# Performance work log

Measured on AMD Instinct MI355X. Metric: run time of the kernel, lower is better.

The kernel has to match this reference:

```python
import jax, jax.numpy as jnp
import numpy as np

B = 4096      # batch
D_IN = 512    # input_dim
D = 256       # d_model
T = 424       # n_targets
L = 6         # num_layers
EPS = 1e-5    # torch LayerNorm default


def _ln(x, g, b):
    m = jnp.mean(x, axis=-1, keepdims=True)
    v = jnp.var(x, axis=-1, keepdims=True)
    return (x - m) * jax.lax.rsqrt(v + EPS) * g + b


def setup_inputs() -> dict:
    key = jax.random.key(0)
    ks = iter(jax.random.split(key, 32))
    r = lambda shape, s=0.05: jax.random.normal(next(ks), shape, dtype=jnp.float32) * s
    return {
        'x': jax.random.normal(next(ks), (B, D_IN), dtype=jnp.float32),
        'proj_W': r((4, D // 4, D_IN)), 'proj_b': r((4, D // 4)),
        'attn_in_W': r((L, 3 * D, D)), 'attn_in_b': r((L, 3 * D)),
        'attn_out_W': r((L, D, D)), 'attn_out_b': r((L, D)),
        'ln_g': jnp.ones((L, D), jnp.float32), 'ln_b': jnp.zeros((L, D), jnp.float32),
        'ff_W1': r((L, 4 * D, D)), 'ff_b1': r((L, 4 * D)),
        'ff_W2': r((L, D, 4 * D)), 'ff_b2': r((L, D)),
        'cross_in_W': r((3 * D, D)), 'cross_in_b': r((3 * D,)),
        'cross_out_W': r((D, D)), 'cross_out_b': r((D,)),
        'tp_W1': r((T, D // 2, D)), 'tp_b1': r((T, D // 2)),
        'tp_ln_g': jnp.ones((T, D // 2), jnp.float32), 'tp_ln_b': jnp.zeros((T, D // 2), jnp.float32),
        'tp_W2': r((T, D // 4, D // 2)), 'tp_b2': r((T, D // 4)),
        'tp_W3': r((T, D // 4)), 'tp_b3': r((T,)),
    }


def reference(x, proj_W, proj_b, attn_in_W, attn_in_b, attn_out_W, attn_out_b,
              ln_g, ln_b, ff_W1, ff_b1, ff_W2, ff_b2,
              cross_in_W, cross_in_b, cross_out_W, cross_out_b,
              tp_W1, tp_b1, tp_ln_g, tp_ln_b, tp_W2, tp_b2, tp_W3, tp_b3):
    # 4 feature projections -> concat == reshape of stacked einsum  [B, 4, D/4] -> [B, D]
    h = jnp.einsum('bd,pkd->bpk', x, proj_W) + proj_b
    h = h.reshape(h.shape[0], D)

    # 6 transformer blocks on seq_len=1: softmax over a single key == 1, so
    # MHA(x,x,x) reduces exactly to out_proj(v_proj(x)); dropout = identity (eval).
    for i in range(L):
        Wv, bv = attn_in_W[i, 2 * D:], attn_in_b[i, 2 * D:]
        attn = (h @ Wv.T + bv) @ attn_out_W[i].T + attn_out_b[i]
        h = _ln(h + attn, ln_g[i], ln_b[i])          # same norm instance reused
        ff = jax.nn.gelu(h @ ff_W1[i].T + ff_b1[i], approximate=False) @ ff_W2[i].T + ff_b2[i]
        h = _ln(h + ff, ln_g[i], ln_b[i])

    # cross-target attention, also seq_len=1 -> v/out projections only
    Wv, bv = cross_in_W[2 * D:], cross_in_b[2 * D:]
    h = h + ((h @ Wv.T + bv) @ cross_out_W.T + cross_out_b)

    # 424 per-target MLP heads, batched as grouped GEMMs
    t = jnp.einsum('bd,tkd->btk', h, tp_W1) + tp_b1          # [B, T, 128]
    t = jax.nn.relu(_ln(t, tp_ln_g, tp_ln_b))
    t = jax.nn.relu(jnp.einsum('btk,tmk->btm', t, tp_W2) + tp_b2)  # [B, T, 64]
    out = jnp.einsum('btm,tm->bt', t, tp_W3) + tp_b3         # [B, T]
    return out
```

## Files before the change

kernel.cpp:

```cpp
#include <hip/hip_runtime.h>
#include <stdint.h>
#include <utility>
#include <type_traits>

using bf16x8 = __attribute__((ext_vector_type(8))) short;
using f32x4  = __attribute__((ext_vector_type(4))) float;

__device__ __forceinline__ f32x4 mfma16(bf16x8 a, bf16x8 b, f32x4 c) {
  return __builtin_amdgcn_mfma_f32_16x16x32_bf16(a, b, c, 0, 0, 0);
}

__device__ __forceinline__ unsigned short f2b_rne(float f) {
  union { float f; unsigned u; } v; v.f = f;
  unsigned r = v.u + 0x7fffu + ((v.u >> 16) & 1u);
  return (unsigned short)(r >> 16);
}

__device__ __forceinline__ void gload16(const void* g, void* l) {
  __builtin_amdgcn_global_load_lds(
      (const __attribute__((address_space(1))) void*)g,
      (__attribute__((address_space(3))) void*)l, 16, 0, 0);
}

template<int N> __device__ __forceinline__ void vmwait() {
  if constexpr (N <= 0)      asm volatile("s_waitcnt vmcnt(0)" ::: "memory");
  else if constexpr (N == 4) asm volatile("s_waitcnt vmcnt(4)" ::: "memory");
  else                       asm volatile("s_waitcnt vmcnt(8)" ::: "memory");
}

template<class F, int... Is>
__device__ __forceinline__ void sfor_impl(F&& f, std::integer_sequence<int, Is...>) {
  (f(std::integral_constant<int, Is>{}), ...);
}
template<int N, class F>
__device__ __forceinline__ void sfor(F&& f) {
  sfor_impl(static_cast<F&&>(f), std::make_integer_sequence<int, N>{});
}

__device__ __forceinline__ void stage_tile(const unsigned short* __restrict__ W, int K,
                                           int col0, int kt, char* slot, int lane) {
#pragma unroll
  for (int i = 0; i < 4; ++i) {
    const int chunk = i * 64 + lane;
    const int ci = chunk >> 4, kc = chunk & 15;
    const unsigned short* src = W + (size_t)(col0 + ci) * K + kt * 128
                                + (((kc * 16) ^ ((ci & 7) << 4)) >> 1);
    gload16(src, slot + i * 1024);
  }
}

template<int NCG, int NKT, int AS, int K>
__device__ __forceinline__ void gemm_pipe(const unsigned short* __restrict__ W, int c0,
                                          const char* __restrict__ abuf,
                                          char* __restrict__ ring, int lane,
                                          f32x4 (&acc)[NCG]) {
  const int r = lane & 15, hi16 = (lane >> 4) << 4;
  const int swz = (r & 7) << 4;
  constexpr int TILES = NCG * NKT;
  stage_tile(W, K, c0, 0, ring, lane);
  if constexpr (TILES > 1)
    stage_tile(W, K, c0 + (1 % NCG) * 16, 1 / NCG, ring + 4096, lane);
  bf16x8 areg[4];
  sfor<TILES>([&](auto tc) {
    constexpr int t = tc.value;
    constexpr int kt = t / NCG, cg = t % NCG;
    vmwait<((t + 2 <= TILES) ? 4 : 0)>();
    __builtin_amdgcn_sched_barrier(0);
    if constexpr (t + 2 < TILES) {
      constexpr int t2 = t + 2;
      stage_tile(W, K, c0 + (t2 % NCG) * 16, t2 / NCG, ring + (t2 % 3) * 4096, lane);
    }
    const char* slot = ring + (t % 3) * 4096;
#pragma unroll
    for (int ksl = 0; ksl < 4; ++ksl) {
      if constexpr (cg == 0)
        areg[ksl] = *reinterpret_cast<const bf16x8*>(
            abuf + r * AS + ((kt * 256 + ksl * 64 + hi16) ^ swz));
      const bf16x8 b = *reinterpret_cast<const bf16x8*>(
          slot + r * 256 + ((ksl * 64 + hi16) ^ swz));
      acc[cg] = mfma16(areg[ksl], b, acc[cg]);
    }
  });
}

__global__ void f2b_kernel(const float* __restrict__ s, unsigned short* __restrict__ d, int n4) {
  int i = blockIdx.x * 256 + threadIdx.x;
  if (i >= n4) return;
  float4 v = reinterpret_cast<const float4*>(s)[i];
  ushort4 o;
  o.x = f2b_rne(v.x); o.y = f2b_rne(v.y); o.z = f2b_rne(v.z); o.w = f2b_rne(v.w);
  reinterpret_cast<ushort4*>(d)[i] = o;
}

__global__ __launch_bounds__(256) void compose_attn(
    const float* __restrict__ aiW, const float* __restrict__ aib,
    const float* __restrict__ aoW, const float* __restrict__ aob,
    const float* __restrict__ ciW, const float* __restrict__ cib,
    const float* __restrict__ coW, const float* __restrict__ cob,
    unsigned short* __restrict__ wEff, float* __restrict__ bEff) {
  const int mat = blockIdx.y;
  const float* Wo = (mat < 6) ? aoW + (size_t)mat * 65536 : coW;
  const float* Wv = (mat < 6) ? aiW + (size_t)mat * 196608 + 131072 : ciW + 131072;
  const float* bv = (mat < 6) ? aib + mat * 768 + 512 : cib + 512;
  const float* bo = (mat < 6) ? aob + mat * 256 : cob;
  unsigned short* Wd = wEff + (size_t)mat * 65536;
  const int m = blockIdx.x * 16 + (threadIdx.x >> 4);
  const int k0 = (threadIdx.x & 15) * 16;
  float c[16] = {};
  for (int j = 0; j < 256; ++j) {
    const float a = Wo[m * 256 + j];
    const float* Br = Wv + j * 256 + k0;
#pragma unroll
    for (int kk = 0; kk < 16; ++kk) c[kk] = fmaf(a, Br[kk], c[kk]);
  }
#pragma unroll
  for (int kk = 0; kk < 16; ++kk) Wd[m * 256 + k0 + kk] = f2b_rne(c[kk]);
  if (blockIdx.x == 0) {
    const int mm = threadIdx.x;
    float s = 0.f;
    for (int j = 0; j < 256; ++j) s = fmaf(Wo[mm * 256 + j], bv[j], s);
    bEff[mat * 256 + mm] = s + bo[mm];
  }
}

__global__ __launch_bounds__(512, 2) void trunk_fused(
    const unsigned short* __restrict__ xb, const unsigned short* __restrict__ pWb,
    const float* __restrict__ projb,
    const unsigned short* __restrict__ wEff, const float* __restrict__ bEff,
    const unsigned short* __restrict__ f1Wb, const float* __restrict__ f1b,
    const unsigned short* __restrict__ f2Wb, const float* __restrict__ f2bp,
    const float* __restrict__ lng, const float* __restrict__ lnb,
    unsigned short* __restrict__ hbf) {
  __shared__ char hbuf[16 * 512];
  __shared__ char gbuf[16 * 2048];
  __shared__ char ringbuf[8 * 12288];
  __shared__ float red[2][16][8];
  const int tid = threadIdx.x, wid = tid >> 6, lane = tid & 63;
  const int r = lane & 15, hi = lane >> 4;
  const int swz = (r & 7) << 4;
  const int row0 = blockIdx.x << 4;
  const int colb = wid * 32;
  char* ring = ringbuf + wid * 12288;

#pragma unroll
  for (int i = 0; i < 2; ++i) {
    const int id = tid + i * 512, row = id >> 6, c8 = id & 63;
    bf16x8 v = *reinterpret_cast<const bf16x8*>(xb + (size_t)(row0 + row) * 512 + c8 * 8);
    *reinterpret_cast<bf16x8*>(gbuf + row * 1024 + ((c8 * 16) ^ ((row & 7) << 4))) = v;
  }
  __syncthreads();

  f32x4 hreg[2];

  auto store_hb = [&]() {
#pragma unroll
    for (int cf = 0; cf < 2; ++cf) {
      const int cb = (colb + cf * 16 + r) * 2;
#pragma unroll
      for (int j = 0; j < 4; ++j) {
        const int row = hi * 4 + j;
        *reinterpret_cast<unsigned short*>(hbuf + row * 512 + (cb ^ ((row & 7) << 4))) =
            f2b_rne(hreg[cf][j]);
      }
    }
  };

  auto ln_apply = [&](float gm0, float gm1, float bb0, float bb1) {
    float sum[4], sq[4];
#pragma unroll
    for (int j = 0; j < 4; ++j) {
      const float v0 = hreg[0][j], v1 = hreg[1][j];
      sum[j] = v0 + v1; sq[j] = v0 * v0 + v1 * v1;
    }
#pragma unroll
    for (int m = 1; m < 16; m <<= 1)
#pragma unroll
      for (int j = 0; j < 4; ++j) {
        sum[j] += __shfl_xor(sum[j], m, 64);
        sq[j]  += __shfl_xor(sq[j],  m, 64);
      }
    if (r == 0)
#pragma unroll
      for (int j = 0; j < 4; ++j) {
        red[0][hi * 4 + j][wid] = sum[j];
        red[1][hi * 4 + j][wid] = sq[j];
      }
    __syncthreads();
#pragma unroll
    for (int j = 0; j < 4; ++j) {
      const int row = hi * 4 + j;
      f32x4 p0 = *reinterpret_cast<const f32x4*>(&red[0][row][0]);
      f32x4 p1 = *reinterpret_cast<const f32x4*>(&red[0][row][4]);
      f32x4 q0 = *reinterpret_cast<const f32x4*>(&red[1][row][0]);
      f32x4 q1 = *reinterpret_cast<const f32x4*>(&red[1][row][4]);
      const float ts = p0[0]+p0[1]+p0[2]+p0[3]+p1[0]+p1[1]+p1[2]+p1[3];
      const float tq = q0[0]+q0[1]+q0[2]+q0[3]+q1[0]+q1[1]+q1[2]+q1[3];
      const float mean = ts * (1.f / 256.f);
      const float rstd = rsqrtf(tq * (1.f / 256.f) - mean * mean + 1e-5f);
      hreg[0][j] = (hreg[0][j] - mean) * rstd * gm0 + bb0;
      hreg[1][j] = (hreg[1][j] - mean) * rstd * gm1 + bb1;
    }
  };

  {
    f32x4 acc[2] = {};
    gemm_pipe<2, 4, 1024, 512>(pWb, colb, gbuf, ring, lane, acc);
    const float bv0 = projb[colb + r], bv1 = projb[colb + 16 + r];
#pragma unroll
    for (int j = 0; j < 4; ++j) { hreg[0][j] = acc[0][j] + bv0; hreg[1][j] = acc[1][j] + bv1; }
  }
  store_hb();
  __syncthreads();

  for (int L = 0; L < 6; ++L) {
    const float gm0 = lng[L * 256 + colb + r],      gm1 = lng[L * 256 + colb + 16 + r];
    const float bb0 = lnb[L * 256 + colb + r],      bb1 = lnb[L * 256 + colb + 16 + r];
    {
      f32x4 acc[2] = {};
      gemm_pipe<2, 2, 512, 256>(wEff + (size_t)L * 65536, colb, hbuf, ring, lane, acc);
      const float be0 = bEff[L * 256 + colb + r], be1 = bEff[L * 256 + colb + 16 + r];
#pragma unroll
      for (int j = 0; j < 4; ++j) { hreg[0][j] += acc[0][j] + be0; hreg[1][j] += acc[1][j] + be1; }
    }
    ln_apply(gm0, gm1, bb0, bb1);
    store_hb();
    __syncthreads();
    {
      f32x4 accf[8] = {};
      gemm_pipe<8, 2, 512, 256>(f1Wb + (size_t)L * 262144, wid * 128, hbuf, ring, lane, accf);
#pragma unroll
      for (int cf = 0; cf < 8; ++cf) {
        const int colw = wid * 128 + cf * 16 + r;
        const float bv = f1b[L * 1024 + colw];
        const int cb = colw * 2;
#pragma unroll
        for (int j = 0; j < 4; ++j) {
          float y = accf[cf][j] + bv;
          y = 0.5f * y * (1.f + erff(y * 0.70710678118654752f));
          const int row = hi * 4 + j;
          *reinterpret_cast<unsigned short*>(gbuf + row * 2048 + (cb ^ ((row & 7) << 4))) = f2b_rne(y);
        }
      }
    }
    __syncthreads();
    {
      f32x4 acc[2] = {};
      gemm_pipe<2, 8, 2048, 1024>(f2Wb + (size_t)L * 262144, colb, gbuf, ring, lane, acc);
      const float be0 = f2bp[L * 256 + colb + r], be1 = f2bp[L * 256 + colb + 16 + r];
#pragma unroll
      for (int j = 0; j < 4; ++j) { hreg[0][j] += acc[0][j] + be0; hreg[1][j] += acc[1][j] + be1; }
    }
    ln_apply(gm0, gm1, bb0, bb1);
    store_hb();
    __syncthreads();
  }

  {
    f32x4 acc[2] = {};
    gemm_pipe<2, 2, 512, 256>(wEff + 6ull * 65536, colb, hbuf, ring, lane, acc);
    const float be0 = bEff[1536 + colb + r], be1 = bEff[1536 + colb + 16 + r];
#pragma unroll
    for (int j = 0; j < 4; ++j) { hreg[0][j] += acc[0][j] + be0; hreg[1][j] += acc[1][j] + be1; }
  }
#pragma unroll
  for (int cf = 0; cf < 2; ++cf)
#pragma unroll
    for (int j = 0; j < 4; ++j)
      hbf[(size_t)(row0 + hi * 4 + j) * 256 + colb + cf * 16 + r] = f2b_rne(hreg[cf][j]);
}

__global__ __launch_bounds__(512, 2) void phase_d2(
    const unsigned short* __restrict__ hbf, const unsigned short* __restrict__ w1b,
    const float* __restrict__ b1, const float* __restrict__ lng, const float* __restrict__ lnb,
    const unsigned short* __restrict__ w2b, const float* __restrict__ b2,
    const float* __restrict__ w3, const float* __restrict__ b3,
    float* __restrict__ out) {
  __shared__ char sm[149504];
  const int tid = threadIdx.x, wid = tid >> 6, lane = tid & 63;
  const int r = lane & 15, hi = lane >> 4;
  const int sw = (r & 7) << 4;
  const int t = blockIdx.y;

  const unsigned short* w1t = w1b + (size_t)t * 32768;
  const unsigned short* w2t = w2b + (size_t)t * 8192;
#pragma unroll
  for (int i = 0; i < 8; ++i) {
    const int id = tid + i * 512;
    const int c = id >> 5, s = id & 31;
    bf16x8 v = *reinterpret_cast<const bf16x8*>(w1t + c * 256 + s * 8);
    *reinterpret_cast<bf16x8*>(sm + c * 512 + ((s * 16) ^ ((c & 7) << 4))) = v;
  }
#pragma unroll
  for (int i = 0; i < 2; ++i) {
    const int id = tid + i * 512;
    const int c = id >> 4, s = id & 15;
    bf16x8 v = *reinterpret_cast<const bf16x8*>(w2t + c * 128 + s * 8);
    *reinterpret_cast<bf16x8*>(sm + 65536 + c * 256 + ((s * 16) ^ ((c & 7) << 4))) = v;
  }
  {
    float v;
    if (tid < 128)      v = b1 [t * 128 + tid];
    else if (tid < 256) v = lng[t * 128 + tid - 128];
    else if (tid < 384) v = lnb[t * 128 + tid - 256];
    else if (tid < 448) v = b2 [t * 64  + tid - 384];
    else                v = w3 [t * 64  + tid - 448];
    reinterpret_cast<float*>(sm + 81920)[tid] = v;
  }
  __syncthreads();

  const float* cb1 = reinterpret_cast<const float*>(sm + 81920);
  const float* cg  = cb1 + 128;
  const float* cbe = cb1 + 256;
  const float* cb2 = cb1 + 384;
  const float* cw3 = cb1 + 448;
  char* t1w = sm + 83968 + wid * 8192;
  const float b3t = b3[t];
  const int token_b0 = blockIdx.x * 1024;

  for (int tile = 0; tile < 2; ++tile) {
    const int B0 = token_b0 + tile * 512 + wid * 64;

    f32x4 acc1[8][4] = {};
    bf16x8 bc[4], bn[4];
#pragma unroll
    for (int bf = 0; bf < 4; ++bf)
      bc[bf] = *reinterpret_cast<const bf16x8*>(hbf + (size_t)(B0 + bf * 16 + r) * 256 + hi * 8);
#pragma unroll
    for (int ks = 0; ks < 8; ++ks) {
      bf16x8 a[8];
#pragma unroll
      for (int cf = 0; cf < 8; ++cf)
        a[cf] = *reinterpret_cast<const bf16x8*>(sm + (cf * 16 + r) * 512 + ((ks * 64 + hi * 16) ^ sw));
      if (ks < 7) {
#pragma unroll
        for (int bf = 0; bf < 4; ++bf)
          bn[bf] = *reinterpret_cast<const bf16x8*>(hbf + (size_t)(B0 + bf * 16 + r) * 256 + (ks + 1) * 32 + hi * 8);
      }
#pragma unroll
      for (int cf = 0; cf < 8; ++cf)
#pragma unroll
        for (int bf = 0; bf < 4; ++bf)
          acc1[cf][bf] = mfma16(a[cf], bc[bf], acc1[cf][bf]);
#pragma unroll
      for (int bf = 0; bf < 4; ++bf) bc[bf] = bn[bf];
    }

#pragma unroll
    for (int cf = 0; cf < 8; ++cf) {
      f32x4 b1v = *reinterpret_cast<const f32x4*>(cb1 + cf * 16 + hi * 4);
#pragma unroll
      for (int bf = 0; bf < 4; ++bf) acc1[cf][bf] += b1v;
    }

    float mu[4], rsd[4];
#pragma unroll
    for (int bf = 0; bf < 4; ++bf) {
      float s = 0.f, s2 = 0.f;
#pragma unroll
      for (int cf = 0; cf < 8; ++cf)
#pragma unroll
        for (int j = 0; j < 4; ++j) { float v = acc1[cf][bf][j]; s += v; s2 += v * v; }
      s  += __shfl_xor(s, 16, 64);  s  += __shfl_xor(s, 32, 64);
      s2 += __shfl_xor(s2, 16, 64); s2 += __shfl_xor(s2, 32, 64);
      const float m = s * (1.f / 128.f);
      mu[bf] = m;
      rsd[bf] = rsqrtf(s2 * (1.f / 128.f) - m * m + 1e-5f);
    }

    f32x4 acc2[4][4] = {};
#pragma unroll
    for (int half = 0; half < 2; ++half) {
#pragma unroll
      for (int cf = 0; cf < 8; ++cf) {
        f32x4 gv = *reinterpret_cast<const f32x4*>(cg  + cf * 16 + hi * 4);
        f32x4 bv = *reinterpret_cast<const f32x4*>(cbe + cf * 16 + hi * 4);
#pragma unroll
        for (int bl = 0; bl < 2; ++bl) {
          const int bf = half * 2 + bl;
          unsigned o01, o23;
          {
            float y0 = fmaxf((acc1[cf][bf][0] - mu[bf]) * rsd[bf] * gv[0] + bv[0], 0.f);
            float y1 = fmaxf((acc1[cf][bf][1] - mu[bf]) * rsd[bf] * gv[1] + bv[1], 0.f);
            float y2 = fmaxf((acc1[cf][bf][2] - mu[bf]) * rsd[bf] * gv[2] + bv[2], 0.f);
            float y3 = fmaxf((acc1[cf][bf][3] - mu[bf]) * rsd[bf] * gv[3] + bv[3], 0.f);
            o01 = (unsigned)f2b_rne(y0) | ((unsigned)f2b_rne(y1) << 16);
            o23 = (unsigned)f2b_rne(y2) | ((unsigned)f2b_rne(y3) << 16);
          }
          uint2 pk; pk.x = o01; pk.y = o23;
          *reinterpret_cast<uint2*>(t1w + (bl * 16 + r) * 256 + ((cf * 32 + hi * 8) ^ sw)) = pk;
        }
      }
#pragma unroll
      for (int ks = 0; ks < 4; ++ks) {
        bf16x8 a2[4];
#pragma unroll
        for (int cf2 = 0; cf2 < 4; ++cf2)
          a2[cf2] = *reinterpret_cast<const bf16x8*>(sm + 65536 + (cf2 * 16 + r) * 256 + ((ks * 64 + hi * 16) ^ sw));
#pragma unroll
        for (int bl = 0; bl < 2; ++bl) {
          bf16x8 bb = *reinterpret_cast<const bf16x8*>(t1w + (bl * 16 + r) * 256 + ((ks * 64 + hi * 16) ^ sw));
#pragma unroll
          for (int cf2 = 0; cf2 < 4; ++cf2)
            acc2[cf2][half * 2 + bl] = mfma16(a2[cf2], bb, acc2[cf2][half * 2 + bl]);
        }
      }
    }

    float s[4] = {0.f, 0.f, 0.f, 0.f};
#pragma unroll
    for (int cf2 = 0; cf2 < 4; ++cf2) {
      f32x4 b2v = *reinterpret_cast<const f32x4*>(cb2 + cf2 * 16 + hi * 4);
      f32x4 w3v = *reinterpret_cast<const f32x4*>(cw3 + cf2 * 16 + hi * 4);
#pragma unroll
      for (int bf = 0; bf < 4; ++bf)
#pragma unroll
        for (int j = 0; j < 4; ++j)
          s[bf] += fmaxf(acc2[cf2][bf][j] + b2v[j], 0.f) * w3v[j];
    }
#pragma unroll
    for (int bf = 0; bf < 4; ++bf) {
      s[bf] += __shfl_xor(s[bf], 16, 64);
      s[bf] += __shfl_xor(s[bf], 32, 64);
      if (hi == 0) out[(size_t)(B0 + bf * 16 + r) * 424 + t] = s[bf] + b3t;
    }
  }
}

extern "C" void kernel_launch(void* const* d_in, const int* in_sizes, int n_in,
                              void* d_out, int out_size, void* d_ws, size_t ws_size,
                              hipStream_t stream) {
  const float* x     = (const float*)d_in[0];
  const float* projW = (const float*)d_in[1];
  const float* projb = (const float*)d_in[2];
  const float* aiW   = (const float*)d_in[3];
  const float* aib   = (const float*)d_in[4];
  const float* aoW   = (const float*)d_in[5];
  const float* aob   = (const float*)d_in[6];
  const float* lng   = (const float*)d_in[7];
  const float* lnbp  = (const float*)d_in[8];
  const float* f1W   = (const float*)d_in[9];
  const float* f1b   = (const float*)d_in[10];
  const float* f2W   = (const float*)d_in[11];
  const float* f2bp  = (const float*)d_in[12];
  const float* ciW   = (const float*)d_in[13];
  const float* cib   = (const float*)d_in[14];
  const float* coW   = (const float*)d_in[15];
  const float* cob   = (const float*)d_in[16];
  const float* tpW1  = (const float*)d_in[17];
  const float* tpb1  = (const float*)d_in[18];
  const float* tplng = (const float*)d_in[19];
  const float* tplnb = (const float*)d_in[20];
  const float* tpW2  = (const float*)d_in[21];
  const float* tpb2  = (const float*)d_in[22];
  const float* tpW3  = (const float*)d_in[23];
  const float* tpb3  = (const float*)d_in[24];
  float* out = (float*)d_out;

  char* ws = (char*)d_ws;
  size_t off = 0;
  auto alloc = [&](size_t n) { char* p = ws + off; off = (off + n + 255) & ~(size_t)255; return p; };
  unsigned short* xb   = (unsigned short*)alloc(4096ull * 512 * 2);
  unsigned short* pWb  = (unsigned short*)alloc(256ull * 512 * 2);
  unsigned short* f1Wb = (unsigned short*)alloc(6ull * 1024 * 256 * 2);
  unsigned short* f2Wb = (unsigned short*)alloc(6ull * 256 * 1024 * 2);
  unsigned short* W1b  = (unsigned short*)alloc(424ull * 128 * 256 * 2);
  unsigned short* W2b  = (unsigned short*)alloc(424ull * 64 * 128 * 2);
  unsigned short* wEff = (unsigned short*)alloc(7ull * 256 * 256 * 2);
  float*          bEff = (float*)alloc(7ull * 256 * 4);
  unsigned short* hbf  = (unsigned short*)alloc(4096ull * 256 * 2);

  auto conv = [&](const float* s, unsigned short* d, size_t n) {
    int n4 = (int)(n >> 2);
    f2b_kernel<<<dim3((n4 + 255) / 256), dim3(256), 0, stream>>>(s, d, n4);
  };
  compose_attn<<<dim3(16, 7), dim3(256), 0, stream>>>(aiW, aib, aoW, aob, ciW, cib, coW, cob, wEff, bEff);
  conv(x, xb, 4096ull * 512);
  conv(projW, pWb, 256ull * 512);
  conv(f1W, f1Wb, 6ull * 1024 * 256);
  conv(f2W, f2Wb, 6ull * 256 * 1024);
  conv(tpW1, W1b, 424ull * 128 * 256);
  conv(tpW2, W2b, 424ull * 64 * 128);

  trunk_fused<<<dim3(256), dim3(512), 0, stream>>>(
      xb, pWb, projb, wEff, bEff, f1Wb, f1b, f2Wb, f2bp, lng, lnbp, hbf);

  phase_d2<<<dim3(4, 424), dim3(512), 0, stream>>>(hbf, W1b, tpb1, tplng, tplnb, W2b, tpb2, tpW3, tpb3, out);
}
```

Before: 523.6 us.

## Shrink trunk weight-staging tiles, deepen head prefetch, add setprio and packed bf16 cvt

The trunk GEMM pipeline now stages 16x32 weight tiles with one 16-byte load per lane into a 4-slot ring, three tiles ahead. This cuts LDS use so the launch bound can ask for 4 blocks per CU instead of 2. In the per-target head kernel, activation prefetch goes two k-steps ahead, MFMA loops are wrapped in s_setprio, and the software bf16 rounding is replaced with the v_cvt_pk_bf16_f32 instruction. The risks are more waitcnt and barrier overhead per MFMA from the smaller tiles, and extra register pressure from the deeper prefetch.

```diff
diff --git a/kernel.cpp b/kernel.cpp
--- a/kernel.cpp
+++ b/kernel.cpp
@@ -16,6 +16,12 @@
   return (unsigned short)(r >> 16);
 }
 
+__device__ __forceinline__ unsigned cvt_pk_bf16(float lo, float hi) {
+  unsigned r;
+  asm("v_cvt_pk_bf16_f32 %0, %1, %2" : "=v"(r) : "v"(lo), "v"(hi));
+  return r;
+}
+
 __device__ __forceinline__ void gload16(const void* g, void* l) {
   __builtin_amdgcn_global_load_lds(
       (const __attribute__((address_space(1))) void*)g,
@@ -24,8 +30,10 @@
 
 template<int N> __device__ __forceinline__ void vmwait() {
   if constexpr (N <= 0)      asm volatile("s_waitcnt vmcnt(0)" ::: "memory");
-  else if constexpr (N == 4) asm volatile("s_waitcnt vmcnt(4)" ::: "memory");
-  else                       asm volatile("s_waitcnt vmcnt(8)" ::: "memory");
+  else if constexpr (N == 1) asm volatile("s_waitcnt vmcnt(1)" ::: "memory");
+  else if constexpr (N == 2) asm volatile("s_waitcnt vmcnt(2)" ::: "memory");
+  else if constexpr (N == 3) asm volatile("s_waitcnt vmcnt(3)" ::: "memory");
+  else                       asm volatile("s_waitcnt vmcnt(4)" ::: "memory");
 }
 
 template<class F, int... Is>
@@ -37,49 +45,42 @@
   sfor_impl(static_cast<F&&>(f), std::make_integer_sequence<int, N>{});
 }
 
-__device__ __forceinline__ void stage_tile(const unsigned short* __restrict__ W, int K,
-                                           int col0, int kt, char* slot, int lane) {
-#pragma unroll
-  for (int i = 0; i < 4; ++i) {
-    const int chunk = i * 64 + lane;
-    const int ci = chunk >> 4, kc = chunk & 15;
-    const unsigned short* src = W + (size_t)(col0 + ci) * K + kt * 128
-                                + (((kc * 16) ^ ((ci & 7) << 4)) >> 1);
-    gload16(src, slot + i * 1024);
-  }
-}
-
-template<int NCG, int NKT, int AS, int K>
-__device__ __forceinline__ void gemm_pipe(const unsigned short* __restrict__ W, int c0,
-                                          const char* __restrict__ abuf,
-                                          char* __restrict__ ring, int lane,
-                                          f32x4 (&acc)[NCG]) {
+__device__ __forceinline__ void stage1(const unsigned short* __restrict__ W, int K,
+                                       int col0, int kt, char* slot, int lane) {
+  const int ci = lane >> 2, kc = lane & 3;
+  const unsigned short* src = W + (size_t)(col0 + ci) * K + kt * 32
+                              + (((kc * 16) ^ ((ci & 3) << 4)) >> 1);
+  gload16(src, slot);
+}
+
+template<int NCG, int AS, int K>
+__device__ __forceinline__ void gemm_pipe2(const unsigned short* __restrict__ W, int c0,
+                                           const char* __restrict__ abuf,
+                                           char* __restrict__ ring, int lane,
+                                           f32x4 (&acc)[NCG]) {
   const int r = lane & 15, hi16 = (lane >> 4) << 4;
-  const int swz = (r & 7) << 4;
+  const int swz7 = (r & 7) << 4, swz3 = (r & 3) << 4;
+  constexpr int NKT = K / 32;
   constexpr int TILES = NCG * NKT;
-  stage_tile(W, K, c0, 0, ring, lane);
-  if constexpr (TILES > 1)
-    stage_tile(W, K, c0 + (1 % NCG) * 16, 1 / NCG, ring + 4096, lane);
-  bf16x8 areg[4];
+  stage1(W, K, c0 + (0 % NCG) * 16, 0 / NCG, ring + 0 * 1024, lane);
+  if constexpr (TILES > 1) stage1(W, K, c0 + (1 % NCG) * 16, 1 / NCG, ring + 1 * 1024, lane);
+  if constexpr (TILES > 2) stage1(W, K, c0 + (2 % NCG) * 16, 2 / NCG, ring + 2 * 1024, lane);
+  bf16x8 areg;
   sfor<TILES>([&](auto tc) {
     constexpr int t = tc.value;
     constexpr int kt = t / NCG, cg = t % NCG;
-    vmwait<((t + 2 <= TILES) ? 4 : 0)>();
+    constexpr int REM = TILES - 1 - t;
+    vmwait<(REM < 2 ? REM : 2)>();
     __builtin_amdgcn_sched_barrier(0);
-    if constexpr (t + 2 < TILES) {
-      constexpr int t2 = t + 2;
-      stage_tile(W, K, c0 + (t2 % NCG) * 16, t2 / NCG, ring + (t2 % 3) * 4096, lane);
-    }
-    const char* slot = ring + (t % 3) * 4096;
-#pragma unroll
-    for (int ksl = 0; ksl < 4; ++ksl) {
-      if constexpr (cg == 0)
-        areg[ksl] = *reinterpret_cast<const bf16x8*>(
-            abuf + r * AS + ((kt * 256 + ksl * 64 + hi16) ^ swz));
-      const bf16x8 b = *reinterpret_cast<const bf16x8*>(
-          slot + r * 256 + ((ksl * 64 + hi16) ^ swz));
-      acc[cg] = mfma16(areg[ksl], b, acc[cg]);
-    }
+    if constexpr (t + 3 < TILES) {
+      constexpr int t3 = t + 3;
+      stage1(W, K, c0 + (t3 % NCG) * 16, t3 / NCG, ring + (t3 & 3) * 1024, lane);
+    }
+    if constexpr (cg == 0)
+      areg = *reinterpret_cast<const bf16x8*>(abuf + r * AS + ((kt * 64 + hi16) ^ swz7));
+    const bf16x8 b = *reinterpret_cast<const bf16x8*>(
+        ring + (t & 3) * 1024 + r * 64 + (hi16 ^ swz3));
+    acc[cg] = mfma16(areg, b, acc[cg]);
   });
 }
 
@@ -123,7 +124,7 @@
   }
 }
 
-__global__ __launch_bounds__(512, 2) void trunk_fused(
+__global__ __launch_bounds__(512, 4) void trunk_fused(
     const unsigned short* __restrict__ xb, const unsigned short* __restrict__ pWb,
     const float* __restrict__ projb,
     const unsigned short* __restrict__ wEff, const float* __restrict__ bEff,
@@ -133,14 +134,13 @@
     unsigned short* __restrict__ hbf) {
   __shared__ char hbuf[16 * 512];
   __shared__ char gbuf[16 * 2048];
-  __shared__ char ringbuf[8 * 12288];
+  __shared__ char ringbuf[8 * 4096];
   __shared__ float red[2][16][8];
   const int tid = threadIdx.x, wid = tid >> 6, lane = tid & 63;
   const int r = lane & 15, hi = lane >> 4;
-  const int swz = (r & 7) << 4;
   const int row0 = blockIdx.x << 4;
   const int colb = wid * 32;
-  char* ring = ringbuf + wid * 12288;
+  char* ring = ringbuf + wid * 4096;
 
 #pragma unroll
   for (int i = 0; i < 2; ++i) {
@@ -204,7 +204,7 @@
 
   {
     f32x4 acc[2] = {};
-    gemm_pipe<2, 4, 1024, 512>(pWb, colb, gbuf, ring, lane, acc);
+    gemm_pipe2<2, 1024, 512>(pWb, colb, gbuf, ring, lane, acc);
     const float bv0 = projb[colb + r], bv1 = projb[colb + 16 + r];
 #pragma unroll
     for (int j = 0; j < 4; ++j) { hreg[0][j] = acc[0][j] + bv0; hreg[1][j] = acc[1][j] + bv1; }
@@ -217,7 +217,7 @@
     const float bb0 = lnb[L * 256 + colb + r],      bb1 = lnb[L * 256 + colb + 16 + r];
     {
       f32x4 acc[2] = {};
-      gemm_pipe<2, 2, 512, 256>(wEff + (size_t)L * 65536, colb, hbuf, ring, lane, acc);
+      gemm_pipe2<2, 512, 256>(wEff + (size_t)L * 65536, colb, hbuf, ring, lane, acc);
       const float be0 = bEff[L * 256 + colb + r], be1 = bEff[L * 256 + colb + 16 + r];
 #pragma unroll
       for (int j = 0; j < 4; ++j) { hreg[0][j] += acc[0][j] + be0; hreg[1][j] += acc[1][j] + be1; }
@@ -227,7 +227,7 @@
     __syncthreads();
     {
       f32x4 accf[8] = {};
-      gemm_pipe<8, 2, 512, 256>(f1Wb + (size_t)L * 262144, wid * 128, hbuf, ring, lane, accf);
+      gemm_pipe2<8, 512, 256>(f1Wb + (size_t)L * 262144, wid * 128, hbuf, ring, lane, accf);
 #pragma unroll
       for (int cf = 0; cf < 8; ++cf) {
         const int colw = wid * 128 + cf * 16 + r;
@@ -245,7 +245,7 @@
     __syncthreads();
     {
       f32x4 acc[2] = {};
-      gemm_pipe<2, 8, 2048, 1024>(f2Wb + (size_t)L * 262144, colb, gbuf, ring, lane, acc);
+      gemm_pipe2<2, 2048, 1024>(f2Wb + (size_t)L * 262144, colb, gbuf, ring, lane, acc);
       const float be0 = f2bp[L * 256 + colb + r], be1 = f2bp[L * 256 + colb + 16 + r];
 #pragma unroll
       for (int j = 0; j < 4; ++j) { hreg[0][j] += acc[0][j] + be0; hreg[1][j] += acc[1][j] + be1; }
@@ -257,7 +257,7 @@
 
   {
     f32x4 acc[2] = {};
-    gemm_pipe<2, 2, 512, 256>(wEff + 6ull * 65536, colb, hbuf, ring, lane, acc);
+    gemm_pipe2<2, 512, 256>(wEff + 6ull * 65536, colb, hbuf, ring, lane, acc);
     const float be0 = bEff[1536 + colb + r], be1 = bEff[1536 + colb + 16 + r];
 #pragma unroll
     for (int j = 0; j < 4; ++j) { hreg[0][j] += acc[0][j] + be0; hreg[1][j] += acc[1][j] + be1; }
@@ -269,7 +269,7 @@
       hbf[(size_t)(row0 + hi * 4 + j) * 256 + colb + cf * 16 + r] = f2b_rne(hreg[cf][j]);
 }
 
-__global__ __launch_bounds__(512, 2) void phase_d2(
+__global__ __launch_bounds__(512, 2) void phase_d3(
     const unsigned short* __restrict__ hbf, const unsigned short* __restrict__ w1b,
     const float* __restrict__ b1, const float* __restrict__ lng, const float* __restrict__ lnb,
     const unsigned short* __restrict__ w2b, const float* __restrict__ b2,
@@ -321,28 +321,33 @@
     const int B0 = token_b0 + tile * 512 + wid * 64;
 
     f32x4 acc1[8][4] = {};
-    bf16x8 bc[4], bn[4];
+    bf16x8 bc[4], bn[4], b2r[4];
 #pragma unroll
     for (int bf = 0; bf < 4; ++bf)
       bc[bf] = *reinterpret_cast<const bf16x8*>(hbf + (size_t)(B0 + bf * 16 + r) * 256 + hi * 8);
 #pragma unroll
+    for (int bf = 0; bf < 4; ++bf)
+      bn[bf] = *reinterpret_cast<const bf16x8*>(hbf + (size_t)(B0 + bf * 16 + r) * 256 + 32 + hi * 8);
+#pragma unroll
     for (int ks = 0; ks < 8; ++ks) {
       bf16x8 a[8];
 #pragma unroll
       for (int cf = 0; cf < 8; ++cf)
         a[cf] = *reinterpret_cast<const bf16x8*>(sm + (cf * 16 + r) * 512 + ((ks * 64 + hi * 16) ^ sw));
-      if (ks < 7) {
+      if (ks < 6) {
 #pragma unroll
         for (int bf = 0; bf < 4; ++bf)
-          bn[bf] = *reinterpret_cast<const bf16x8*>(hbf + (size_t)(B0 + bf * 16 + r) * 256 + (ks + 1) * 32 + hi * 8);
-      }
+          b2r[bf] = *reinterpret_cast<const bf16x8*>(hbf + (size_t)(B0 + bf * 16 + r) * 256 + (ks + 2) * 32 + hi * 8);
+      }
+      __builtin_amdgcn_s_setprio(1);
 #pragma unroll
       for (int cf = 0; cf < 8; ++cf)
 #pragma unroll
         for (int bf = 0; bf < 4; ++bf)
           acc1[cf][bf] = mfma16(a[cf], bc[bf], acc1[cf][bf]);
-#pragma unroll
-      for (int bf = 0; bf < 4; ++bf) bc[bf] = bn[bf];
+      __builtin_amdgcn_s_setprio(0);
+#pragma unroll
+      for (int bf = 0; bf < 4; ++bf) { bc[bf] = bn[bf]; bn[bf] = b2r[bf]; }
     }
 
 #pragma unroll
@@ -377,16 +382,13 @@
 #pragma unroll
         for (int bl = 0; bl < 2; ++bl) {
           const int bf = half * 2 + bl;
-          unsigned o01, o23;
-          {
-            float y0 = fmaxf((acc1[cf][bf][0] - mu[bf]) * rsd[bf] * gv[0] + bv[0], 0.f);
-            float y1 = fmaxf((acc1[cf][bf][1] - mu[bf]) * rsd[bf] * gv[1] + bv[1], 0.f);
-            float y2 = fmaxf((acc1[cf][bf][2] - mu[bf]) * rsd[bf] * gv[2] + bv[2], 0.f);
-            float y3 = fmaxf((acc1[cf][bf][3] - mu[bf]) * rsd[bf] * gv[3] + bv[3], 0.f);
-            o01 = (unsigned)f2b_rne(y0) | ((unsigned)f2b_rne(y1) << 16);
-            o23 = (unsigned)f2b_rne(y2) | ((unsigned)f2b_rne(y3) << 16);
-          }
-          uint2 pk; pk.x = o01; pk.y = o23;
+          float y0 = fmaxf((acc1[cf][bf][0] - mu[bf]) * rsd[bf] * gv[0] + bv[0], 0.f);
+          float y1 = fmaxf((acc1[cf][bf][1] - mu[bf]) * rsd[bf] * gv[1] + bv[1], 0.f);
+          float y2 = fmaxf((acc1[cf][bf][2] - mu[bf]) * rsd[bf] * gv[2] + bv[2], 0.f);
+          float y3 = fmaxf((acc1[cf][bf][3] - mu[bf]) * rsd[bf] * gv[3] + bv[3], 0.f);
+          uint2 pk;
+          pk.x = cvt_pk_bf16(y0, y1);
+          pk.y = cvt_pk_bf16(y2, y3);
           *reinterpret_cast<uint2*>(t1w + (bl * 16 + r) * 256 + ((cf * 32 + hi * 8) ^ sw)) = pk;
         }
       }
@@ -396,6 +398,7 @@
 #pragma unroll
         for (int cf2 = 0; cf2 < 4; ++cf2)
           a2[cf2] = *reinterpret_cast<const bf16x8*>(sm + 65536 + (cf2 * 16 + r) * 256 + ((ks * 64 + hi * 16) ^ sw));
+        __builtin_amdgcn_s_setprio(1);
 #pragma unroll
         for (int bl = 0; bl < 2; ++bl) {
           bf16x8 bb = *reinterpret_cast<const bf16x8*>(t1w + (bl * 16 + r) * 256 + ((ks * 64 + hi * 16) ^ sw));
@@ -403,6 +406,7 @@
           for (int cf2 = 0; cf2 < 4; ++cf2)
             acc2[cf2][half * 2 + bl] = mfma16(a2[cf2], bb, acc2[cf2][half * 2 + bl]);
         }
+        __builtin_amdgcn_s_setprio(0);
       }
     }
 
@@ -484,5 +488,5 @@
   trunk_fused<<<dim3(256), dim3(512), 0, stream>>>(
       xb, pWb, projb, wEff, bEff, f1Wb, f1b, f2Wb, f2bp, lng, lnbp, hbf);
 
-  phase_d2<<<dim3(4, 424), dim3(512), 0, stream>>>(hbf, W1b, tpb1, tplng, tplnb, W2b, tpb2, tpW3, tpb3, out);
-}
+  phase_d3<<<dim3(4, 424), dim3(512), 0, stream>>>(hbf, W1b, tpb1, tplng, tplnb, W2b, tpb2, tpW3, tpb3, out);
+}
```

New measurement: 570.3 us. +8.9%, slower.
